# Kernel tuning notes

Hardware: AMD Instinct MI355X
Metric: run time of the kernel (lower is better)

Reference implementation:

```python
import jax, jax.numpy as jnp
import numpy as np

# Standard NF4 codebook (bitsandbytes values)
NF4_LEVELS = jnp.array([
    -1.0, -0.6961928009986877, -0.5250730514526367, -0.39491748809814453,
    -0.28444138169288635, -0.18477343022823334, -0.09105003625154495, 0.0,
    0.07958029955625534, 0.16093020141124725, 0.24611230194568634,
    0.33791524171829224, 0.44070982933044434, 0.5626170039176941,
    0.7229568362236023, 1.0], dtype=jnp.float32)

GROUP_SIZE = 64
SCALING = 32.0 / 8.0  # alpha / r


def setup_inputs() -> dict:
    key = jax.random.key(0)
    k0, k1, k2, k3, k4, k5 = jax.random.split(key, 6)
    B, S, IN, OUT, R = 4, 2048, 4096, 4096, 8
    x = jax.random.normal(k0, (B, S, IN), dtype=jnp.float32)
    q_weight = jax.random.randint(k1, (OUT, IN), 0, 16, dtype=jnp.int32)
    # per-group absmax scales (positive)
    q_scale = jax.random.uniform(k2, (OUT * IN // GROUP_SIZE,),
                                 dtype=jnp.float32, minval=0.005, maxval=0.05)
    bias = jax.random.normal(k3, (OUT,), dtype=jnp.float32) * 0.01
    lora_A = jax.random.normal(k4, (R, IN), dtype=jnp.float32) * 0.01
    lora_B = jax.random.normal(k5, (OUT, R), dtype=jnp.float32) * 0.01
    return {"x": x, "q_weight": q_weight, "q_scale": q_scale,
            "bias": bias, "lora_A": lora_A, "lora_B": lora_B}


def reference(x, q_weight, q_scale, bias, lora_A, lora_B):
    OUT, IN = q_weight.shape
    # NF4 dequantize: codebook lookup, then per-group scale (groups of 64 along flat weight)
    w = NF4_LEVELS[q_weight].reshape(-1, GROUP_SIZE) * q_scale[:, None]
    w = w.reshape(OUT, IN).astype(x.dtype)  # [OUT, IN]
    # base linear: x [B,S,IN] @ w.T -> [B,S,OUT]
    base = jnp.einsum('bsi,oi->bso', x, w) + bias
    # LoRA low-rank path (dropout p=0 -> identity)
    lora = jnp.einsum('bsr,or->bso', jnp.einsum('bsi,ri->bsr', x, lora_A), lora_B)
    return base + SCALING * lora
```

## Files before the change

### kernel.cpp

```cpp
#include <hip/hip_runtime.h>
#include <hip/hip_bf16.h>
#include <stdint.h>

typedef int i32x4 __attribute__((ext_vector_type(4)));

#define AS1 __attribute__((address_space(1)))
#define AS3 __attribute__((address_space(3)))

__constant__ float c_nf4[16] = {
    -1.0f, -0.6961928009986877f, -0.5250730514526367f, -0.39491748809814453f,
    -0.28444138169288635f, -0.18477343022823334f, -0.09105003625154495f, 0.0f,
    0.07958029955625534f, 0.16093020141124725f, 0.24611230194568634f,
    0.33791524171829224f, 0.44070982933044434f, 0.5626170039176941f,
    0.7229568362236023f, 1.0f};

__global__ __launch_bounds__(256) void k_prepq(
    const int* __restrict__ q, const float* __restrict__ scale,
    const float* __restrict__ lA, const float* __restrict__ lB,
    const float* __restrict__ x, int8_t* __restrict__ Wq,
    int8_t* __restrict__ Xq, float* __restrict__ sw, float* __restrict__ sx,
    int IN, int R, int OUT, int nrows) {
  const int lane = threadIdx.x & 63;
  const int row = blockIdx.x * 4 + (threadIdx.x >> 6);
  if (row >= nrows) return;

  float v[64];

  if (row < OUT) {
    const long rbase = (long)row * IN;
    float br[8];
#pragma unroll
    for (int r = 0; r < 8; ++r) br[r] = (r < R) ? 4.0f * lB[row * R + r] : 0.0f;
#pragma unroll
    for (int c = 0; c < 4; ++c) {
      const int e0 = c * 1024 + lane * 16;
      const float s = scale[(rbase + e0) >> 6];
      const int* qp = q + rbase + e0;
#pragma unroll
      for (int u = 0; u < 4; ++u) {
        int4 qa = *(const int4*)(qp + u * 4);
        v[c * 16 + u * 4 + 0] = c_nf4[qa.x & 15] * s;
        v[c * 16 + u * 4 + 1] = c_nf4[qa.y & 15] * s;
        v[c * 16 + u * 4 + 2] = c_nf4[qa.z & 15] * s;
        v[c * 16 + u * 4 + 3] = c_nf4[qa.w & 15] * s;
      }
      for (int r = 0; r < R; ++r) {
        const float* ap = lA + (long)r * IN + e0;
#pragma unroll
        for (int u = 0; u < 4; ++u) {
          float4 a = *(const float4*)(ap + u * 4);
          v[c * 16 + u * 4 + 0] += br[r] * a.x;
          v[c * 16 + u * 4 + 1] += br[r] * a.y;
          v[c * 16 + u * 4 + 2] += br[r] * a.z;
          v[c * 16 + u * 4 + 3] += br[r] * a.w;
        }
      }
    }
  } else {
    const float* xp = x + (long)(row - OUT) * IN;
#pragma unroll
    for (int c = 0; c < 4; ++c) {
      const int e0 = c * 1024 + lane * 16;
#pragma unroll
      for (int u = 0; u < 4; ++u) {
        float4 a = *(const float4*)(xp + e0 + u * 4);
        v[c * 16 + u * 4 + 0] = a.x; v[c * 16 + u * 4 + 1] = a.y;
        v[c * 16 + u * 4 + 2] = a.z; v[c * 16 + u * 4 + 3] = a.w;
      }
    }
  }

  float am = 0.0f;
#pragma unroll
  for (int i = 0; i < 64; ++i) am = fmaxf(am, fabsf(v[i]));
#pragma unroll
  for (int m = 32; m >= 1; m >>= 1) am = fmaxf(am, __shfl_xor(am, m));
  am = fmaxf(am, 1e-30f);
  const float inv = 127.0f / am;

  int8_t* dst = (row < OUT) ? (Wq + (long)row * IN) : (Xq + (long)(row - OUT) * IN);
#pragma unroll
  for (int c = 0; c < 4; ++c) {
    union { int8_t b[16]; int4 p; } pk;
#pragma unroll
    for (int i = 0; i < 16; ++i)
      pk.b[i] = (int8_t)(int)rintf(v[c * 16 + i] * inv);
    *(int4*)(dst + c * 1024 + lane * 16) = pk.p;
  }
  if (lane == 0) {
    if (row < OUT) sw[row] = am * (1.0f / 127.0f);
    else sx[row - OUT] = am * (1.0f / 127.0f);
  }
}

__global__ __launch_bounds__(512, 2) void k_gemm_256(
    const int8_t* __restrict__ Xq, const int8_t* __restrict__ Wq,
    const float* __restrict__ sx, const float* __restrict__ sw,
    const float* __restrict__ bias, float* __restrict__ out,
    int M, int N, int K) {
  __shared__ char smem[131072];
  const int tid = threadIdx.x;
  const int wid = tid >> 6;
  const int lane = tid & 63;
  const int wr = wid >> 2;
  const int wc = wid & 3;
  const int wcl = wc & 1;
  const int l15 = lane & 15;
  const int l16 = lane >> 4;

  const int kflip = (l15 & 4) ? 64 : 0;
  const int lowx = ((l16 ^ (l15 & 3)) << 4);
  const int baseA0 = wr * 16384 + l15 * 128 + lowx + kflip;
  const int baseA1 = wr * 16384 + l15 * 128 + lowx + (64 ^ kflip);
  const int baseB0 = 65536 + (wc >> 1) * 16384 + wcl * 8192 + l15 * 128 + lowx + kflip;
  const int baseB1 = baseB0 + (64 ^ kflip) - kflip;

  int bid = blockIdx.x;
  const int nwg = gridDim.x;
  if ((nwg & 7) == 0) { const int cpx = nwg >> 3; bid = (bid & 7) * cpx + (bid >> 3); }
  const int nbn = N >> 8;
  const int m0 = (bid / nbn) << 8;
  const int n0 = (bid % nbn) << 8;

  int rowj[2], gcj[2];
#pragma unroll
  for (int j = 0; j < 2; ++j) {
    const int lo = wid * 2048 + j * 1024 + lane * 16;
    const int row = lo >> 7;
    const int ls = lo ^ ((row & 7) << 4);
    rowj[j] = row;
    gcj[j] = ls & 127;
  }
  const size_t halfstep = (size_t)128 * K;
  const int8_t* pSA0[2]; const int8_t* pSA1[2];
  const int8_t* pSB0[2]; const int8_t* pSB1[2];
#pragma unroll
  for (int j = 0; j < 2; ++j) {
    pSA0[j] = Xq + (size_t)(m0 + rowj[j]) * K + gcj[j];
    pSA1[j] = pSA0[j] + halfstep;
    pSB0[j] = Wq + (size_t)(n0 + rowj[j]) * K + gcj[j];
    pSB1[j] = pSB0[j] + halfstep;
  }

#define ST_A(bufl, h, coff)                                                          \
  {                                                                                  \
    __builtin_amdgcn_global_load_lds((const AS1 void*)(pSA##h[0] + (coff)),          \
        (AS3 void*)(smem + (bufl) * 32768 + (h) * 16384 + wid * 2048), 16, 0, 0);    \
    __builtin_amdgcn_global_load_lds((const AS1 void*)(pSA##h[1] + (coff)),          \
        (AS3 void*)(smem + (bufl) * 32768 + (h) * 16384 + wid * 2048 + 1024),        \
        16, 0, 0);                                                                   \
  }
#define ST_B(bufl, h, coff)                                                          \
  {                                                                                  \
    __builtin_amdgcn_global_load_lds((const AS1 void*)(pSB##h[0] + (coff)),          \
        (AS3 void*)(smem + 65536 + (bufl) * 32768 + (h) * 16384 + wid * 2048),       \
        16, 0, 0);                                                                   \
    __builtin_amdgcn_global_load_lds((const AS1 void*)(pSB##h[1] + (coff)),          \
        (AS3 void*)(smem + 65536 + (bufl) * 32768 + (h) * 16384 + wid * 2048 + 1024),\
        16, 0, 0);                                                                   \
  }

  i32x4 afA[4][2], afB[4][2], b0[2][2], b1[2][2];
  i32x4 acc[8][4];
#pragma unroll
  for (int i = 0; i < 8; ++i)
#pragma unroll
    for (int j = 0; j < 4; ++j) acc[i][j] = (i32x4)0;

#define RD_A(bufl, mq, dst)                                                          \
  _Pragma("unroll") for (int ii = 0; ii < 4; ++ii) {                                 \
    dst[ii][0] = *(const i32x4*)(smem + baseA0 +                                     \
                                 ((bufl) * 32768 + (mq) * 8192 + ii * 2048));        \
    dst[ii][1] = *(const i32x4*)(smem + baseA1 +                                     \
                                 ((bufl) * 32768 + (mq) * 8192 + ii * 2048));        \
  }
#define RD_B(bufl, q, arr)                                                           \
  _Pragma("unroll") for (int jj = 0; jj < 2; ++jj) {                                 \
    arr[jj][0] = *(const i32x4*)(smem + baseB0 +                                     \
                                 ((bufl) * 32768 + (q) * 4096 + jj * 2048));         \
    arr[jj][1] = *(const i32x4*)(smem + baseB1 +                                     \
                                 ((bufl) * 32768 + (q) * 4096 + jj * 2048));         \
  }
#define MFMA_Q(mq, q, A, arr)                                                        \
  _Pragma("unroll") for (int kk = 0; kk < 2; ++kk)                                   \
  _Pragma("unroll") for (int ii = 0; ii < 4; ++ii)                                   \
  _Pragma("unroll") for (int jj = 0; jj < 2; ++jj)                                   \
      acc[(mq)*4+ii][(q)*2+jj] = __builtin_amdgcn_mfma_i32_16x16x64_i8(              \
          A[ii][kk], arr[jj][kk], acc[(mq)*4+ii][(q)*2+jj], 0, 0, 0);

#define BAR __builtin_amdgcn_s_barrier()
#define PRIO1 __builtin_amdgcn_s_setprio(1)
#define PRIO0 __builtin_amdgcn_s_setprio(0)
#define LGK0                                               \
  {                                                        \
    asm volatile("s_waitcnt lgkmcnt(0)" ::: "memory");     \
    __builtin_amdgcn_sched_barrier(0);                     \
  }
#define VM4 asm volatile("s_waitcnt vmcnt(4)" ::: "memory")
#define VM8 asm volatile("s_waitcnt vmcnt(8)" ::: "memory")

#define SUBTILE(bufl, SC)                                                            \
                                                                             \
  LGK0; PRIO1; MFMA_Q(0, 0, afA, b0) PRIO0;                                          \
  RD_B(bufl, 1, b1)                                                                  \
  BAR;                                                                               \
                                                                             \
  LGK0; PRIO1; MFMA_Q(0, 1, afA, b1) PRIO0;                                          \
  RD_A(bufl, 1, afB)                                                                 \
  BAR;                                                                               \
                                   \
  LGK0; PRIO1; MFMA_Q(1, 0, afB, b0) PRIO0;                                          \
  ST_B(bufl, 0, SC) ST_B(bufl, 1, SC)                                                \
  VM4;                                                                               \
  BAR;                                                                               \
            \
  PRIO1; MFMA_Q(1, 1, afB, b1) PRIO0;                                                \
  ST_A(bufl, 0, SC) ST_A(bufl, 1, SC)                                                \
  RD_A((bufl) ^ 1, 0, afA)                                                           \
  RD_B((bufl) ^ 1, 0, b0)                                                            \
  BAR;

  const int NT = K >> 7;

  ST_A(0, 0, 0) ST_A(0, 1, 0) ST_B(0, 0, 0) ST_B(0, 1, 0)
  ST_A(1, 0, 128) ST_A(1, 1, 128) ST_B(1, 0, 128) ST_B(1, 1, 128)
  VM8;
  BAR;
  RD_A(0, 0, afA)
  RD_B(0, 0, b0)
#pragma unroll
  for (int j = 0; j < 2; ++j) { pSA0[j] += 256; pSA1[j] += 256; pSB0[j] += 256; pSB1[j] += 256; }

  for (int t = 0; t < NT; t += 2) {
    SUBTILE(0, 0)
    SUBTILE(1, 128)
    if (t + 4 < NT) {
#pragma unroll
      for (int j = 0; j < 2; ++j) { pSA0[j] += 256; pSA1[j] += 256; pSB0[j] += 256; pSB1[j] += 256; }
    }
  }

  float bv[4], swc[4];
#pragma unroll
  for (int nf = 0; nf < 4; ++nf) {
    const int col = n0 + wc * 64 + nf * 16 + l15;
    bv[nf] = bias[col];
    swc[nf] = sw[col];
  }
#pragma unroll
  for (int mi = 0; mi < 8; ++mi) {
    const int rbase = m0 + wr * 128 + mi * 16 + l16 * 4;
    const float4 sx4 = *(const float4*)(sx + rbase);
#pragma unroll
    for (int nf = 0; nf < 4; ++nf) {
      const int col = n0 + wc * 64 + nf * 16 + l15;
      const float s0 = sx4.x * swc[nf], s1 = sx4.y * swc[nf];
      const float s2 = sx4.z * swc[nf], s3 = sx4.w * swc[nf];
      out[(size_t)(rbase + 0) * N + col] = (float)acc[mi][nf][0] * s0 + bv[nf];
      out[(size_t)(rbase + 1) * N + col] = (float)acc[mi][nf][1] * s1 + bv[nf];
      out[(size_t)(rbase + 2) * N + col] = (float)acc[mi][nf][2] * s2 + bv[nf];
      out[(size_t)(rbase + 3) * N + col] = (float)acc[mi][nf][3] * s3 + bv[nf];
    }
  }
#undef ST_A
#undef ST_B
#undef RD_A
#undef RD_B
#undef MFMA_Q
#undef BAR
#undef PRIO1
#undef PRIO0
#undef LGK0
#undef VM4
#undef VM8
#undef SUBTILE
}

extern "C" void kernel_launch(void* const* d_in, const int* in_sizes, int n_in,
                              void* d_out, int out_size, void* d_ws, size_t ws_size,
                              hipStream_t stream) {
  const float* x = (const float*)d_in[0];
  const int* qw = (const int*)d_in[1];
  const float* qs = (const float*)d_in[2];
  const float* bias = (const float*)d_in[3];
  const float* lA = (const float*)d_in[4];
  const float* lB = (const float*)d_in[5];
  float* out = (float*)d_out;

  const int OUT = in_sizes[3];
  const long qn = (long)in_sizes[1];
  const int IN = (int)(qn / OUT);
  const int R = in_sizes[5] / OUT;
  const long xn = (long)in_sizes[0];
  const int M = (int)(xn / IN);
  const int N = OUT, K = IN;

  int8_t* Wq = (int8_t*)d_ws;
  int8_t* Xq = Wq + qn;
  float* sw = (float*)(((uintptr_t)(Xq + xn) + 15) & ~(uintptr_t)15);
  float* sx = sw + OUT;

  const int nrows = OUT + M;
  k_prepq<<<(nrows + 3) / 4, 256, 0, stream>>>(qw, qs, lA, lB, x, Wq, Xq, sw, sx,
                                               IN, R, OUT, nrows);

  dim3 grid((M / 256) * (N / 256));
  k_gemm_256<<<grid, 512, 0, stream>>>(Xq, Wq, sx, sw, bias, out, M, N, K);
}
```

Measured before the change: 200.4 us.

## Shrink int8 GEMM macro-tile from 256x256 to 128x128 with 4 waves

Replaces the 512-thread 256x256 int8 MFMA GEMM kernel with a 256-thread 128x128 variant that uses 64KB of LDS. The staging loads, fragment reads and epilogue are rewritten to match: each wave now owns a 64x64 output tile and issues four strided global-to-LDS loads per operand. The smaller tile gives a larger grid and lower LDS per block, which may improve occupancy and tail balance. In exchange it roughly halves operand reuse per byte loaded, so global and LDS traffic rise. The vmcnt wait counts are left unchanged, which could alter pipelining correctness.

```diff
diff --git a/kernel.cpp b/kernel.cpp
--- a/kernel.cpp
+++ b/kernel.cpp
@@ -93,100 +93,79 @@
   }
 }
 
-__global__ __launch_bounds__(512, 2) void k_gemm_256(
+__global__ __launch_bounds__(256, 2) void k_gemm_128(
     const int8_t* __restrict__ Xq, const int8_t* __restrict__ Wq,
     const float* __restrict__ sx, const float* __restrict__ sw,
     const float* __restrict__ bias, float* __restrict__ out,
     int M, int N, int K) {
-  __shared__ char smem[131072];
+  __shared__ char smem[65536];
   const int tid = threadIdx.x;
   const int wid = tid >> 6;
   const int lane = tid & 63;
-  const int wr = wid >> 2;
-  const int wc = wid & 3;
-  const int wcl = wc & 1;
+  const int wr = wid >> 1;
+  const int wc = wid & 1;
   const int l15 = lane & 15;
   const int l16 = lane >> 4;
 
   const int kflip = (l15 & 4) ? 64 : 0;
   const int lowx = ((l16 ^ (l15 & 3)) << 4);
-  const int baseA0 = wr * 16384 + l15 * 128 + lowx + kflip;
-  const int baseA1 = wr * 16384 + l15 * 128 + lowx + (64 ^ kflip);
-  const int baseB0 = 65536 + (wc >> 1) * 16384 + wcl * 8192 + l15 * 128 + lowx + kflip;
+  const int baseA0 = wr * 8192 + l15 * 128 + lowx + kflip;
+  const int baseA1 = wr * 8192 + l15 * 128 + lowx + (64 ^ kflip);
+  const int baseB0 = 32768 + wc * 8192 + l15 * 128 + lowx + kflip;
   const int baseB1 = baseB0 + (64 ^ kflip) - kflip;
 
   int bid = blockIdx.x;
   const int nwg = gridDim.x;
   if ((nwg & 7) == 0) { const int cpx = nwg >> 3; bid = (bid & 7) * cpx + (bid >> 3); }
-  const int nbn = N >> 8;
-  const int m0 = (bid / nbn) << 8;
-  const int n0 = (bid % nbn) << 8;
-
-  int rowj[2], gcj[2];
-#pragma unroll
-  for (int j = 0; j < 2; ++j) {
-    const int lo = wid * 2048 + j * 1024 + lane * 16;
-    const int row = lo >> 7;
-    const int ls = lo ^ ((row & 7) << 4);
-    rowj[j] = row;
-    gcj[j] = ls & 127;
-  }
-  const size_t halfstep = (size_t)128 * K;
-  const int8_t* pSA0[2]; const int8_t* pSA1[2];
-  const int8_t* pSB0[2]; const int8_t* pSB1[2];
-#pragma unroll
-  for (int j = 0; j < 2; ++j) {
-    pSA0[j] = Xq + (size_t)(m0 + rowj[j]) * K + gcj[j];
-    pSA1[j] = pSA0[j] + halfstep;
-    pSB0[j] = Wq + (size_t)(n0 + rowj[j]) * K + gcj[j];
-    pSB1[j] = pSB0[j] + halfstep;
-  }
-
-#define ST_A(bufl, h, coff)                                                          \
-  {                                                                                  \
-    __builtin_amdgcn_global_load_lds((const AS1 void*)(pSA##h[0] + (coff)),          \
-        (AS3 void*)(smem + (bufl) * 32768 + (h) * 16384 + wid * 2048), 16, 0, 0);    \
-    __builtin_amdgcn_global_load_lds((const AS1 void*)(pSA##h[1] + (coff)),          \
-        (AS3 void*)(smem + (bufl) * 32768 + (h) * 16384 + wid * 2048 + 1024),        \
-        16, 0, 0);                                                                   \
-  }
-#define ST_B(bufl, h, coff)                                                          \
-  {                                                                                  \
-    __builtin_amdgcn_global_load_lds((const AS1 void*)(pSB##h[0] + (coff)),          \
-        (AS3 void*)(smem + 65536 + (bufl) * 32768 + (h) * 16384 + wid * 2048),       \
-        16, 0, 0);                                                                   \
-    __builtin_amdgcn_global_load_lds((const AS1 void*)(pSB##h[1] + (coff)),          \
-        (AS3 void*)(smem + 65536 + (bufl) * 32768 + (h) * 16384 + wid * 2048 + 1024),\
-        16, 0, 0);                                                                   \
-  }
-
-  i32x4 afA[4][2], afB[4][2], b0[2][2], b1[2][2];
-  i32x4 acc[8][4];
-#pragma unroll
-  for (int i = 0; i < 8; ++i)
+  const int nbn = N >> 7;
+  const int m0 = (bid / nbn) << 7;
+  const int n0 = (bid % nbn) << 7;
+
+  const int lo = wid * 1024 + lane * 16;
+  const int srow = lo >> 7;
+  const int sls = lo ^ ((srow & 7) << 4);
+  const int sgc = sls & 127;
+  const size_t k32 = (size_t)32 * K;
+  const int8_t* pSA = Xq + (size_t)(m0 + srow) * K + sgc;
+  const int8_t* pSB = Wq + (size_t)(n0 + srow) * K + sgc;
+
+#define ST_A(bufl, coff)                                                             \
+  _Pragma("unroll") for (int c = 0; c < 4; ++c)                                      \
+      __builtin_amdgcn_global_load_lds((const AS1 void*)(pSA + c * k32 + (coff)),    \
+          (AS3 void*)(smem + (bufl) * 16384 + c * 4096 + wid * 1024), 16, 0, 0);
+#define ST_B(bufl, coff)                                                             \
+  _Pragma("unroll") for (int c = 0; c < 4; ++c)                                      \
+      __builtin_amdgcn_global_load_lds((const AS1 void*)(pSB + c * k32 + (coff)),    \
+          (AS3 void*)(smem + 32768 + (bufl) * 16384 + c * 4096 + wid * 1024),        \
+          16, 0, 0);
+
+  i32x4 afA01[2][2], afA23[2][2], b01[2][2], b23[2][2];
+  i32x4 acc[4][4];
+#pragma unroll
+  for (int i = 0; i < 4; ++i)
 #pragma unroll
     for (int j = 0; j < 4; ++j) acc[i][j] = (i32x4)0;
 
-#define RD_A(bufl, mq, dst)                                                          \
-  _Pragma("unroll") for (int ii = 0; ii < 4; ++ii) {                                 \
+#define RD_A(bufl, ih, dst)                                                          \
+  _Pragma("unroll") for (int ii = 0; ii < 2; ++ii) {                                 \
     dst[ii][0] = *(const i32x4*)(smem + baseA0 +                                     \
-                                 ((bufl) * 32768 + (mq) * 8192 + ii * 2048));        \
+                                 ((bufl) * 16384 + (ih) * 4096 + ii * 2048));        \
     dst[ii][1] = *(const i32x4*)(smem + baseA1 +                                     \
-                                 ((bufl) * 32768 + (mq) * 8192 + ii * 2048));        \
-  }
-#define RD_B(bufl, q, arr)                                                           \
+                                 ((bufl) * 16384 + (ih) * 4096 + ii * 2048));        \
+  }
+#define RD_B(bufl, jh, arr)                                                          \
   _Pragma("unroll") for (int jj = 0; jj < 2; ++jj) {                                 \
     arr[jj][0] = *(const i32x4*)(smem + baseB0 +                                     \
-                                 ((bufl) * 32768 + (q) * 4096 + jj * 2048));         \
+                                 ((bufl) * 16384 + (jh) * 4096 + jj * 2048));        \
     arr[jj][1] = *(const i32x4*)(smem + baseB1 +                                     \
-                                 ((bufl) * 32768 + (q) * 4096 + jj * 2048));         \
-  }
-#define MFMA_Q(mq, q, A, arr)                                                        \
+                                 ((bufl) * 16384 + (jh) * 4096 + jj * 2048));        \
+  }
+#define MFMA_Q(ih, jh, A, arr)                                                       \
   _Pragma("unroll") for (int kk = 0; kk < 2; ++kk)                                   \
-  _Pragma("unroll") for (int ii = 0; ii < 4; ++ii)                                   \
+  _Pragma("unroll") for (int ii = 0; ii < 2; ++ii)                                   \
   _Pragma("unroll") for (int jj = 0; jj < 2; ++jj)                                   \
-      acc[(mq)*4+ii][(q)*2+jj] = __builtin_amdgcn_mfma_i32_16x16x64_i8(              \
-          A[ii][kk], arr[jj][kk], acc[(mq)*4+ii][(q)*2+jj], 0, 0, 0);
+      acc[(ih)*2+ii][(jh)*2+jj] = __builtin_amdgcn_mfma_i32_16x16x64_i8(             \
+          A[ii][kk], arr[jj][kk], acc[(ih)*2+ii][(jh)*2+jj], 0, 0, 0);
 
 #define BAR __builtin_amdgcn_s_barrier()
 #define PRIO1 __builtin_amdgcn_s_setprio(1)
@@ -201,43 +180,39 @@
 
 #define SUBTILE(bufl, SC)                                                            \
                                                                              \
-  LGK0; PRIO1; MFMA_Q(0, 0, afA, b0) PRIO0;                                          \
-  RD_B(bufl, 1, b1)                                                                  \
+  LGK0; PRIO1; MFMA_Q(0, 0, afA01, b01) PRIO0;                                       \
+  RD_B(bufl, 1, b23)                                                                 \
   BAR;                                                                               \
                                                                              \
-  LGK0; PRIO1; MFMA_Q(0, 1, afA, b1) PRIO0;                                          \
-  RD_A(bufl, 1, afB)                                                                 \
+  LGK0; PRIO1; MFMA_Q(0, 1, afA01, b23) PRIO0;                                       \
+  RD_A(bufl, 1, afA23)                                                               \
   BAR;                                                                               \
                                    \
-  LGK0; PRIO1; MFMA_Q(1, 0, afB, b0) PRIO0;                                          \
-  ST_B(bufl, 0, SC) ST_B(bufl, 1, SC)                                                \
+  LGK0; PRIO1; MFMA_Q(1, 0, afA23, b01) PRIO0;                                       \
+  ST_B(bufl, SC)                                                                     \
   VM4;                                                                               \
   BAR;                                                                               \
-            \
-  PRIO1; MFMA_Q(1, 1, afB, b1) PRIO0;                                                \
-  ST_A(bufl, 0, SC) ST_A(bufl, 1, SC)                                                \
-  RD_A((bufl) ^ 1, 0, afA)                                                           \
-  RD_B((bufl) ^ 1, 0, b0)                                                            \
+             \
+  PRIO1; MFMA_Q(1, 1, afA23, b23) PRIO0;                                             \
+  ST_A(bufl, SC)                                                                     \
+  RD_A((bufl) ^ 1, 0, afA01)                                                         \
+  RD_B((bufl) ^ 1, 0, b01)                                                           \
   BAR;
 
   const int NT = K >> 7;
 
-  ST_A(0, 0, 0) ST_A(0, 1, 0) ST_B(0, 0, 0) ST_B(0, 1, 0)
-  ST_A(1, 0, 128) ST_A(1, 1, 128) ST_B(1, 0, 128) ST_B(1, 1, 128)
+  ST_A(0, 0) ST_B(0, 0)
+  ST_A(1, 128) ST_B(1, 128)
   VM8;
   BAR;
-  RD_A(0, 0, afA)
-  RD_B(0, 0, b0)
-#pragma unroll
-  for (int j = 0; j < 2; ++j) { pSA0[j] += 256; pSA1[j] += 256; pSB0[j] += 256; pSB1[j] += 256; }
+  RD_A(0, 0, afA01)
+  RD_B(0, 0, b01)
+  pSA += 256; pSB += 256;
 
   for (int t = 0; t < NT; t += 2) {
     SUBTILE(0, 0)
     SUBTILE(1, 128)
-    if (t + 4 < NT) {
-#pragma unroll
-      for (int j = 0; j < 2; ++j) { pSA0[j] += 256; pSA1[j] += 256; pSB0[j] += 256; pSB1[j] += 256; }
-    }
+    if (t + 4 < NT) { pSA += 256; pSB += 256; }
   }
 
   float bv[4], swc[4];
@@ -248,8 +223,8 @@
     swc[nf] = sw[col];
   }
 #pragma unroll
-  for (int mi = 0; mi < 8; ++mi) {
-    const int rbase = m0 + wr * 128 + mi * 16 + l16 * 4;
+  for (int mi = 0; mi < 4; ++mi) {
+    const int rbase = m0 + wr * 64 + mi * 16 + l16 * 4;
     const float4 sx4 = *(const float4*)(sx + rbase);
 #pragma unroll
     for (int nf = 0; nf < 4; ++nf) {
@@ -304,6 +279,6 @@
   k_prepq<<<(nrows + 3) / 4, 256, 0, stream>>>(qw, qs, lA, lB, x, Wq, Xq, sw, sx,
                                                IN, R, OUT, nrows);
 
-  dim3 grid((M / 256) * (N / 256));
-  k_gemm_256<<<grid, 512, 0, stream>>>(Xq, Wq, sx, sw, bias, out, M, N, K);
+  dim3 grid((M / 128) * (N / 128));
+  k_gemm_128<<<grid, 256, 0, stream>>>(Xq, Wq, sx, sw, bias, out, M, N, K);
 }
```

Result: slower. 252.5 us (+26.0%).
